# Kernel tuning notes

Hardware: AMD Instinct MI355X
Metric: run time of the kernel (lower is better)

The kernel has to match this reference:

```python
import jax, jax.numpy as jnp
import numpy as np

B, T, C, H = 2, 2048, 1024, 16
D = C // H  # head dim = 64

def setup_inputs() -> dict:
    key = jax.random.key(0)
    ks = jax.random.split(key, 5)
    s = 1.0 / np.sqrt(C)
    return {
        "x": jax.random.normal(ks[0], (B, T, C), jnp.float32),
        "Wq": jax.random.normal(ks[1], (C, C), jnp.float32) * s,
        "Wk": jax.random.normal(ks[2], (C, C), jnp.float32) * s,
        "Wv": jax.random.normal(ks[3], (C, C), jnp.float32) * s,
        "Wo": jax.random.normal(ks[4], (C, C), jnp.float32) * s,
    }

def reference(x, Wq, Wk, Wv, Wo):
    # torch Linear: y = x @ W.T  (weights stored [out, in])
    def proj(W):
        h = jnp.einsum('btc,oc->bto', x, W)
        return h.reshape(B, T, H, D).transpose(0, 2, 1, 3)  # [B,H,T,D]
    q, k, v = proj(Wq), proj(Wk), proj(Wv)
    scale = 1.0 / np.sqrt(D)
    att = jnp.einsum('bhqd,bhkd->bhqk', q, k) * scale  # [B,H,T,T]
    causal = jnp.tril(jnp.ones((T, T), bool))
    att = jnp.where(causal[None, None], att, -jnp.inf)
    att = jax.nn.softmax(att, axis=-1)
    y = jnp.einsum('bhqk,bhkd->bhqd', att, v)  # [B,H,T,D]
    y = y.transpose(0, 2, 1, 3).reshape(B, T, C)
    return jnp.einsum('btc,oc->bto', y, Wo)
```

## Files before the change

kernel.cpp:

```cpp
#include <hip/hip_runtime.h>
#include <math.h>

typedef short bf16x8 __attribute__((ext_vector_type(8)));
typedef float f32x4 __attribute__((ext_vector_type(4)));
typedef float f32x16 __attribute__((ext_vector_type(16)));
typedef int int2v __attribute__((ext_vector_type(2)));

constexpr int Bc = 2, Tc = 2048, Cc = 1024, Hc = 16, Dc = 64;
constexpr int Mc = Bc * Tc;

#if __has_builtin(__builtin_amdgcn_exp2f)
#define EXP2(x) __builtin_amdgcn_exp2f(x)
#else
#define EXP2(x) exp2f(x)
#endif

#define SBAR() do { asm volatile("" ::: "memory"); \
                    __builtin_amdgcn_s_barrier();   \
                    asm volatile("" ::: "memory"); } while (0)

__device__ __forceinline__ unsigned short f2bf(float f) {
    union { float f; unsigned u; } v; v.f = f;
    unsigned r = v.u + 0x7fffu + ((v.u >> 16) & 1u);
    return (unsigned short)(r >> 16);
}

__device__ __forceinline__ float bf2f(unsigned short u) {
    union { unsigned u; float f; } v; v.u = (unsigned)u << 16; return v.f;
}

__device__ __forceinline__ unsigned cvt_pk_bf16(float lo, float hi) {
    unsigned r;
    asm("v_cvt_pk_bf16_f32 %0, %1, %2" : "=v"(r) : "v"(lo), "v"(hi));
    return r;
}

__device__ __forceinline__ void gload16(const void* g, void* l) {
    __builtin_amdgcn_global_load_lds(
        (const __attribute__((address_space(1))) void*)g,
        (__attribute__((address_space(3))) void*)l, 16, 0, 0);
}

__global__ __launch_bounds__(256)
void cast_bf16(const float* __restrict__ in, unsigned short* __restrict__ out, int n8) {
    int i = blockIdx.x * 256 + threadIdx.x;
    if (i >= n8) return;
    const float4* p = (const float4*)in;
    float4 a = p[i * 2], b = p[i * 2 + 1];
    union { unsigned short u[8]; bf16x8 v; } r;
    r.u[0] = f2bf(a.x); r.u[1] = f2bf(a.y); r.u[2] = f2bf(a.z); r.u[3] = f2bf(a.w);
    r.u[4] = f2bf(b.x); r.u[5] = f2bf(b.y); r.u[6] = f2bf(b.z); r.u[7] = f2bf(b.w);
    *(bf16x8*)(out + i * 8) = r.v;
}

__global__ __launch_bounds__(256)
void cast_w4(const float* __restrict__ a, const float* __restrict__ b,
             const float* __restrict__ c, const float* __restrict__ d,
             unsigned short* __restrict__ oa, unsigned short* __restrict__ ob,
             unsigned short* __restrict__ oc, unsigned short* __restrict__ od) {
    const float* src = blockIdx.y == 0 ? a : blockIdx.y == 1 ? b : blockIdx.y == 2 ? c : d;
    unsigned short* dst = blockIdx.y == 0 ? oa : blockIdx.y == 1 ? ob : blockIdx.y == 2 ? oc : od;
    int i = blockIdx.x * 256 + threadIdx.x;
    const float4* p = (const float4*)src;
    float4 x = p[i * 2], y = p[i * 2 + 1];
    union { unsigned short u[8]; bf16x8 v; } r;
    r.u[0] = f2bf(x.x); r.u[1] = f2bf(x.y); r.u[2] = f2bf(x.z); r.u[3] = f2bf(x.w);
    r.u[4] = f2bf(y.x); r.u[5] = f2bf(y.y); r.u[6] = f2bf(y.z); r.u[7] = f2bf(y.w);
    *(bf16x8*)(dst + i * 8) = r.v;
}

__global__ __launch_bounds__(256)
void gemm_qkv(const unsigned short* __restrict__ A,
              const unsigned short* __restrict__ Wq,
              const unsigned short* __restrict__ Wk,
              const unsigned short* __restrict__ Wv,
              unsigned short* __restrict__ Qo,
              unsigned short* __restrict__ Ko,
              unsigned short* __restrict__ Vo) {
    __shared__ unsigned short As[128 * 32];
    __shared__ unsigned short Bs[64 * 32];
    const int t = threadIdx.x;
    const int lane = t & 63, l15 = lane & 15, l4 = lane >> 4;
    const int w = t >> 6, wr = w >> 1, wc = w & 1;
    const int seg = blockIdx.y >> 4;
    const unsigned short* W = seg == 0 ? Wq : seg == 1 ? Wk : Wv;
    const int m0 = blockIdx.x * 128, n0 = (blockIdx.y & 15) * 64;

    f32x4 acc[4][2] = {};

    for (int k0 = 0; k0 < Cc; k0 += 32) {
        __syncthreads();
        #pragma unroll
        for (int it = 0; it < 2; ++it) {
            int c = t + it * 256;
            int row = c >> 2, ko = (c & 3) << 3;
            gload16(A + (size_t)(m0 + row) * Cc + k0 + ko, As + c * 8);
        }
        {
            int row = t >> 2, ko = (t & 3) << 3;
            gload16(W + (size_t)(n0 + row) * Cc + k0 + ko, Bs + t * 8);
        }
        __syncthreads();
        bf16x8 af[4], bfr[2];
        #pragma unroll
        for (int i = 0; i < 4; ++i)
            af[i] = *(const bf16x8*)(As + ((wr * 64 + i * 16 + l15) * 32 + l4 * 8));
        #pragma unroll
        for (int j = 0; j < 2; ++j)
            bfr[j] = *(const bf16x8*)(Bs + ((wc * 32 + j * 16 + l15) * 32 + l4 * 8));
        #pragma unroll
        for (int i = 0; i < 4; ++i)
            #pragma unroll
            for (int j = 0; j < 2; ++j)
                acc[i][j] = __builtin_amdgcn_mfma_f32_16x16x32_bf16(af[i], bfr[j], acc[i][j], 0, 0, 0);
    }

    const float qscale = 0.18033688011112042f;
    const int r0 = wr * 64 + (l4 << 2);
    const int c0 = wc * 32 + l15;
    #pragma unroll
    for (int i = 0; i < 4; ++i)
        #pragma unroll
        for (int j = 0; j < 2; ++j)
            #pragma unroll
            for (int r = 0; r < 4; ++r) {
                int row = m0 + r0 + i * 16 + r;
                int col = n0 + c0 + j * 16;
                float v = acc[i][j][r];
                int bb = row >> 11, tt = row & (Tc - 1);
                int hh = col >> 6, dd = col & 63;
                if (seg == 0)
                    Qo[((((size_t)bb * Hc + hh) * Tc + tt) << 6) + dd] = f2bf(v * qscale);
                else if (seg == 1)
                    Ko[((((size_t)bb * Hc + hh) * Tc + tt) << 6) + dd] = f2bf(v);
                else
                    Vo[(((size_t)bb * Hc + hh) * Dc + dd) * Tc + tt] = f2bf(v);
            }
}

__global__ __launch_bounds__(256)
void gemm_out(const unsigned short* __restrict__ A,
              const unsigned short* __restrict__ W,
              float* __restrict__ outp) {
    __shared__ unsigned short As[64 * 32];
    __shared__ unsigned short Bs[64 * 32];
    const int t = threadIdx.x;
    const int lane = t & 63, l15 = lane & 15, l4 = lane >> 4;
    const int w = t >> 6, wr = w >> 1, wc = w & 1;
    const int m0 = blockIdx.x * 64, n0 = blockIdx.y * 64;

    f32x4 acc[2][2] = {};

    for (int k0 = 0; k0 < Cc; k0 += 32) {
        __syncthreads();
        {
            int row = t >> 2, ko = (t & 3) << 3;
            gload16(A + (size_t)(m0 + row) * Cc + k0 + ko, As + t * 8);
            gload16(W + (size_t)(n0 + row) * Cc + k0 + ko, Bs + t * 8);
        }
        __syncthreads();
        bf16x8 af[2], bfr[2];
        #pragma unroll
        for (int i = 0; i < 2; ++i)
            af[i] = *(const bf16x8*)(As + ((wr * 32 + i * 16 + l15) * 32 + l4 * 8));
        #pragma unroll
        for (int j = 0; j < 2; ++j)
            bfr[j] = *(const bf16x8*)(Bs + ((wc * 32 + j * 16 + l15) * 32 + l4 * 8));
        #pragma unroll
        for (int i = 0; i < 2; ++i)
            #pragma unroll
            for (int j = 0; j < 2; ++j)
                acc[i][j] = __builtin_amdgcn_mfma_f32_16x16x32_bf16(af[i], bfr[j], acc[i][j], 0, 0, 0);
    }

    const int r0 = wr * 32 + (l4 << 2);
    const int c0 = wc * 32 + l15;
    #pragma unroll
    for (int i = 0; i < 2; ++i)
        #pragma unroll
        for (int j = 0; j < 2; ++j)
            #pragma unroll
            for (int r = 0; r < 4; ++r)
                outp[(size_t)(m0 + r0 + i * 16 + r) * Cc + n0 + c0 + j * 16] = acc[i][j][r];
}

__device__ __constant__ unsigned char JOBS[48] = {
    159, 223, 222, 15, 158, 157, 221, 220, 14, 156,
    155, 219, 218, 13, 154, 153, 217, 216, 12, 152,
    151, 215, 214, 11, 150, 149, 213, 212, 10, 148,
    147, 211, 210,  9, 146, 145, 209, 208,  8, 144,
      7,   6,   5,  4,   3,   2,   1,   0
};

__global__ __launch_bounds__(128)
void attn_mfma(const unsigned short* __restrict__ Q,
               const unsigned short* __restrict__ K,
               const unsigned short* __restrict__ Vt,
               unsigned short* __restrict__ Y,
               unsigned short* __restrict__ P1,
               float* __restrict__ mlf) {
    __shared__ unsigned short Ks[2][64 * 64];
    __shared__ unsigned short Vs[2][64 * 64];

    const int t = threadIdx.x, lane = t & 63, w = t >> 6;
    const int l31 = lane & 31, h = lane >> 5;
    const int bh = blockIdx.x;
    const int bb = bh >> 4, hh = bh & 15;

    const unsigned char job = JOBS[blockIdx.y];
    const int c = job & 31;
    const bool split = job & 128;
    const int half = (job >> 6) & 1;
    const int ntile = c + 1, smid = ntile >> 1;
    const int kb0 = (split && half) ? smid : 0;
    const int kb1 = (split && !half) ? smid : ntile;

    const int qbase = c * 64 + w * 32;
    const int q = qbase + l31;

    const unsigned short* Qp = Q + (size_t)bh * Tc * Dc;
    const unsigned short* Kp = K + (size_t)bh * Tc * Dc;
    const unsigned short* Vp = Vt + (size_t)bh * Dc * Tc;

    bf16x8 qf[4];
    #pragma unroll
    for (int kc = 0; kc < 4; ++kc)
        qf[kc] = *(const bf16x8*)(Qp + (size_t)q * 64 + kc * 16 + h * 8);

    f32x16 ot[2] = {};
    float m = -INFINITY, lsum = 0.f;

    auto stage = [&](int kb, int buf) {
        #pragma unroll
        for (int it = 0; it < 4; ++it) {
            int idx = t + it * 128;
            int row = idx >> 3, slot = idx & 7;
            int ss = slot ^ (row & 7);
            gload16(Kp + (size_t)(kb * 64 + row) * 64 + ss * 8, &Ks[buf][idx * 8]);
            gload16(Vp + (size_t)row * Tc + kb * 64 + ss * 8, &Vs[buf][idx * 8]);
        }
    };

    stage(kb0, 0);
    if (kb0 + 1 < kb1) stage(kb0 + 1, 1);

    for (int kb = kb0; kb < kb1; ++kb) {
        const int cur = (kb - kb0) & 1;
        if (kb + 1 < kb1) asm volatile("s_waitcnt vmcnt(8)" ::: "memory");
        else              asm volatile("s_waitcnt vmcnt(0)" ::: "memory");
        SBAR();

        f32x16 st[2] = {};
        __builtin_amdgcn_s_setprio(1);
        #pragma unroll
        for (int nt = 0; nt < 2; ++nt) {
            int key = nt * 32 + l31;
            #pragma unroll
            for (int kc = 0; kc < 4; ++kc) {
                int boff = (kc * 32 + h * 16) ^ ((key & 7) << 4);
                bf16x8 kf = *(const bf16x8*)(&Ks[cur][((key << 7) + boff) >> 1]);
                st[nt] = __builtin_amdgcn_mfma_f32_32x32x16_bf16(kf, qf[kc], st[nt], 0, 0, 0);
            }
        }
        __builtin_amdgcn_s_setprio(0);

        if (kb * 64 + 63 > qbase) {
            #pragma unroll
            for (int nt = 0; nt < 2; ++nt)
                #pragma unroll
                for (int r = 0; r < 16; ++r) {
                    int key = kb * 64 + nt * 32 + (r & 3) + 8 * (r >> 2) + 4 * h;
                    if (key > q) st[nt][r] = -1e30f;
                }
        }

        float mx[16];
        #pragma unroll
        for (int r = 0; r < 16; ++r) mx[r] = fmaxf(st[0][r], st[1][r]);
        #pragma unroll
        for (int s2 = 8; s2 > 0; s2 >>= 1)
            #pragma unroll
            for (int r = 0; r < s2; ++r) mx[r] = fmaxf(mx[r], mx[r + s2]);
        float tmax = fmaxf(mx[0], __shfl_xor(mx[0], 32));

        if (__any(tmax > m + 8.f)) {
            float mn = fmaxf(m, tmax);
            float al = EXP2(m - mn);
            m = mn;
            lsum *= al;
            #pragma unroll
            for (int dt = 0; dt < 2; ++dt)
                #pragma unroll
                for (int r = 0; r < 16; ++r) ot[dt][r] *= al;
        }

        float psa[4] = {0.f, 0.f, 0.f, 0.f};
        #pragma unroll
        for (int nt = 0; nt < 2; ++nt)
            #pragma unroll
            for (int r = 0; r < 16; ++r) {
                float p = EXP2(st[nt][r] - m);
                st[nt][r] = p;
                psa[r & 3] += p;
            }
        lsum += (psa[0] + psa[1]) + (psa[2] + psa[3]);

        #pragma unroll
        for (int nt = 0; nt < 2; ++nt) {
            unsigned a0 = cvt_pk_bf16(st[nt][0],  st[nt][1]);
            unsigned b0 = cvt_pk_bf16(st[nt][4],  st[nt][5]);
            unsigned a1 = cvt_pk_bf16(st[nt][2],  st[nt][3]);
            unsigned b1 = cvt_pk_bf16(st[nt][6],  st[nt][7]);
            int2v r0 = __builtin_amdgcn_permlane32_swap((int)a0, (int)b0, false, false);
            int2v r1 = __builtin_amdgcn_permlane32_swap((int)a1, (int)b1, false, false);
            union { unsigned u[4]; bf16x8 v; } pf0, pf1;
            pf0.u[0] = r0.x; pf0.u[1] = r1.x; pf0.u[2] = r0.y; pf0.u[3] = r1.y;
            unsigned c0 = cvt_pk_bf16(st[nt][8],  st[nt][9]);
            unsigned d0 = cvt_pk_bf16(st[nt][12], st[nt][13]);
            unsigned c1 = cvt_pk_bf16(st[nt][10], st[nt][11]);
            unsigned d1 = cvt_pk_bf16(st[nt][14], st[nt][15]);
            int2v r2 = __builtin_amdgcn_permlane32_swap((int)c0, (int)d0, false, false);
            int2v r3 = __builtin_amdgcn_permlane32_swap((int)c1, (int)d1, false, false);
            pf1.u[0] = r2.x; pf1.u[1] = r3.x; pf1.u[2] = r2.y; pf1.u[3] = r3.y;

            __builtin_amdgcn_s_setprio(1);
            #pragma unroll
            for (int dt = 0; dt < 2; ++dt) {
                int d = dt * 32 + l31;
                int v0off = (nt * 64 + h * 16) ^ ((d & 7) << 4);
                bf16x8 vf0 = *(const bf16x8*)(&Vs[cur][((d << 7) + v0off) >> 1]);
                ot[dt] = __builtin_amdgcn_mfma_f32_32x32x16_bf16(vf0, pf0.v, ot[dt], 0, 0, 0);
            }
            #pragma unroll
            for (int dt = 0; dt < 2; ++dt) {
                int d = dt * 32 + l31;
                int v1off = (nt * 64 + 32 + h * 16) ^ ((d & 7) << 4);
                bf16x8 vf1 = *(const bf16x8*)(&Vs[cur][((d << 7) + v1off) >> 1]);
                ot[dt] = __builtin_amdgcn_mfma_f32_32x32x16_bf16(vf1, pf1.v, ot[dt], 0, 0, 0);
            }
            __builtin_amdgcn_s_setprio(0);
        }

        SBAR();
        if (kb + 2 < kb1) stage(kb + 2, cur);
    }

    float lf = lsum + __shfl_xor(lsum, 32);
    unsigned short* dst = (split && half) ? P1 : Y;
    float inv = split ? 1.f : 1.f / lf;
    size_t base = ((size_t)bb * Tc + q) * Cc + hh * 64;
    #pragma unroll
    for (int dt = 0; dt < 2; ++dt)
        #pragma unroll
        for (int rg = 0; rg < 4; ++rg) {
            int d0 = dt * 32 + rg * 8 + 4 * h;
            ushort4 s4;
            s4.x = f2bf(ot[dt][rg * 4 + 0] * inv);
            s4.y = f2bf(ot[dt][rg * 4 + 1] * inv);
            s4.z = f2bf(ot[dt][rg * 4 + 2] * inv);
            s4.w = f2bf(ot[dt][rg * 4 + 3] * inv);
            *(ushort4*)(dst + base + d0) = s4;
        }
    if (split && h == 0) {
        int ridx = bh * 1024 + (q - 1024);
        mlf[ridx + (half ? 65536 : 0)]     = m;
        mlf[ridx + (half ? 98304 : 32768)] = lf;
    }
}

__global__ __launch_bounds__(256)
void attn_combine(unsigned short* __restrict__ Y,
                  const unsigned short* __restrict__ P1,
                  const float* __restrict__ mlf) {
    int tid = blockIdx.x * 256 + threadIdx.x;
    int ridx = tid >> 3;
    int d0 = (tid & 7) * 8;
    int bh = ridx >> 10, qq = ridx & 1023;
    int bb = bh >> 4, hh = bh & 15;
    int q = 1024 + qq;
    size_t off = ((size_t)bb * Tc + q) * Cc + hh * 64 + d0;
    float m0 = mlf[ridx], l0 = mlf[ridx + 32768];
    float m1 = mlf[ridx + 65536], l1 = mlf[ridx + 98304];
    float M = fmaxf(m0, m1);
    float a0 = exp2f(m0 - M), a1 = exp2f(m1 - M);
    float inv = 1.f / (l0 * a0 + l1 * a1);
    union { unsigned short u[8]; bf16x8 v; } y0, y1, r;
    y0.v = *(const bf16x8*)(Y + off);
    y1.v = *(const bf16x8*)(P1 + off);
    #pragma unroll
    for (int j = 0; j < 8; ++j)
        r.u[j] = f2bf((bf2f(y0.u[j]) * a0 + bf2f(y1.u[j]) * a1) * inv);
    *(bf16x8*)(Y + off) = r.v;
}

extern "C" void kernel_launch(void* const* d_in, const int* in_sizes, int n_in,
                              void* d_out, int out_size, void* d_ws, size_t ws_size,
                              hipStream_t stream) {
    const float* x  = (const float*)d_in[0];
    const float* Wq = (const float*)d_in[1];
    const float* Wk = (const float*)d_in[2];
    const float* Wv = (const float*)d_in[3];
    const float* Wo = (const float*)d_in[4];

    unsigned short* ws = (unsigned short*)d_ws;
    const size_t nX = (size_t)Mc * Cc;
    const size_t nW = (size_t)Cc * Cc;
    size_t off = 0;
    unsigned short* xb  = ws + off; off += nX;
    unsigned short* Wqb = ws + off; off += nW;
    unsigned short* Wkb = ws + off; off += nW;
    unsigned short* Wvb = ws + off; off += nW;
    unsigned short* Wob = ws + off; off += nW;
    unsigned short* Qw  = ws + off; off += nX;
    unsigned short* Kw  = ws + off; off += nX;
    unsigned short* Vtw = ws + off; off += nX;
    unsigned short* Yb  = ws + off; off += nX;

    dim3 blk(256);
    cast_bf16<<<dim3((int)(nX / 8 / 256)), blk, 0, stream>>>(x, xb, (int)(nX / 8));
    cast_w4<<<dim3(512, 4), blk, 0, stream>>>(Wq, Wk, Wv, Wo, Wqb, Wkb, Wvb, Wob);

    gemm_qkv<<<dim3(Mc / 128, 48), blk, 0, stream>>>(xb, Wqb, Wkb, Wvb, Qw, Kw, Vtw);

    unsigned short* P1 = xb;
    float* mlf = (float*)Wqb;
    attn_mfma<<<dim3(Bc * Hc, 48), dim3(128), 0, stream>>>(Qw, Kw, Vtw, Yb, P1, mlf);
    attn_combine<<<dim3(1024), blk, 0, stream>>>(Yb, P1, mlf);

    gemm_out<<<dim3(Mc / 64, Cc / 64), blk, 0, stream>>>(Yb, Wob, (float*)d_out);
}
```

Baseline: 133.3 us.

## Split attention KV range into up to three parts and widen QKV GEMM tiles

The attention kernel now splits the causal KV range of each query tile into one, two or three partitions depending on tile depth. It launches 72 jobs per head ordered longest-first to balance work across CUs, and the combine kernel merges two or three partial outputs with their max/sum statistics. Separately, the QKV GEMM tile grows from 128x64 to 128x128 so each A tile is reused more and fewer blocks are launched. This adds extra partial-output traffic and combine work in exchange for better load balance, and it repurposes more workspace buffers (Wqb, Wvb) as scratch.

```diff
diff --git a/kernel.cpp b/kernel.cpp
--- a/kernel.cpp
+++ b/kernel.cpp
@@ -78,15 +78,15 @@
               unsigned short* __restrict__ Ko,
               unsigned short* __restrict__ Vo) {
     __shared__ unsigned short As[128 * 32];
-    __shared__ unsigned short Bs[64 * 32];
+    __shared__ unsigned short Bs[128 * 32];
     const int t = threadIdx.x;
     const int lane = t & 63, l15 = lane & 15, l4 = lane >> 4;
     const int w = t >> 6, wr = w >> 1, wc = w & 1;
-    const int seg = blockIdx.y >> 4;
+    const int seg = blockIdx.y >> 3;
     const unsigned short* W = seg == 0 ? Wq : seg == 1 ? Wk : Wv;
-    const int m0 = blockIdx.x * 128, n0 = (blockIdx.y & 15) * 64;
-
-    f32x4 acc[4][2] = {};
+    const int m0 = blockIdx.x * 128, n0 = (blockIdx.y & 7) * 128;
+
+    f32x4 acc[4][4] = {};
 
     for (int k0 = 0; k0 < Cc; k0 += 32) {
         __syncthreads();
@@ -95,33 +95,30 @@
             int c = t + it * 256;
             int row = c >> 2, ko = (c & 3) << 3;
             gload16(A + (size_t)(m0 + row) * Cc + k0 + ko, As + c * 8);
-        }
-        {
-            int row = t >> 2, ko = (t & 3) << 3;
-            gload16(W + (size_t)(n0 + row) * Cc + k0 + ko, Bs + t * 8);
+            gload16(W + (size_t)(n0 + row) * Cc + k0 + ko, Bs + c * 8);
         }
         __syncthreads();
-        bf16x8 af[4], bfr[2];
+        bf16x8 af[4], bfr[4];
         #pragma unroll
         for (int i = 0; i < 4; ++i)
             af[i] = *(const bf16x8*)(As + ((wr * 64 + i * 16 + l15) * 32 + l4 * 8));
         #pragma unroll
-        for (int j = 0; j < 2; ++j)
-            bfr[j] = *(const bf16x8*)(Bs + ((wc * 32 + j * 16 + l15) * 32 + l4 * 8));
+        for (int j = 0; j < 4; ++j)
+            bfr[j] = *(const bf16x8*)(Bs + ((wc * 64 + j * 16 + l15) * 32 + l4 * 8));
         #pragma unroll
         for (int i = 0; i < 4; ++i)
             #pragma unroll
-            for (int j = 0; j < 2; ++j)
+            for (int j = 0; j < 4; ++j)
                 acc[i][j] = __builtin_amdgcn_mfma_f32_16x16x32_bf16(af[i], bfr[j], acc[i][j], 0, 0, 0);
     }
 
     const float qscale = 0.18033688011112042f;
     const int r0 = wr * 64 + (l4 << 2);
-    const int c0 = wc * 32 + l15;
+    const int c0 = wc * 64 + l15;
     #pragma unroll
     for (int i = 0; i < 4; ++i)
         #pragma unroll
-        for (int j = 0; j < 2; ++j)
+        for (int j = 0; j < 4; ++j)
             #pragma unroll
             for (int r = 0; r < 4; ++r) {
                 int row = m0 + r0 + i * 16 + r;
@@ -184,12 +181,16 @@
                 outp[(size_t)(m0 + r0 + i * 16 + r) * Cc + n0 + c0 + j * 16] = acc[i][j][r];
 }
 
-__device__ __constant__ unsigned char JOBS[48] = {
-    159, 223, 222, 15, 158, 157, 221, 220, 14, 156,
-    155, 219, 218, 13, 154, 153, 217, 216, 12, 152,
-    151, 215, 214, 11, 150, 149, 213, 212, 10, 148,
-    147, 211, 210,  9, 146, 145, 209, 208,  8, 144,
-      7,   6,   5,  4,   3,   2,   1,   0
+__device__ __constant__ unsigned char JOBS[72] = {
+    125,126,122,
+    124,120,121,116,117,118,113,114,110,
+    112,108,109,104,105,106,101,102, 98,
+    100, 96, 97, 92, 93, 94, 89, 90, 86, 60, 61, 57, 28,
+     88, 84, 85, 80, 81, 82, 77, 78, 74, 56, 52, 53, 49, 24,
+     76, 72, 73, 68, 69, 70, 65, 66, 48, 44, 45, 41, 20,
+     64, 40, 36, 37, 33, 16,
+     32, 12,
+      8,  4,  0
 };
 
 __global__ __launch_bounds__(128)
@@ -198,6 +199,7 @@
                const unsigned short* __restrict__ Vt,
                unsigned short* __restrict__ Y,
                unsigned short* __restrict__ P1,
+               unsigned short* __restrict__ P2,
                float* __restrict__ mlf) {
     __shared__ unsigned short Ks[2][64 * 64];
     __shared__ unsigned short Vs[2][64 * 64];
@@ -208,12 +210,13 @@
     const int bb = bh >> 4, hh = bh & 15;
 
     const unsigned char job = JOBS[blockIdx.y];
-    const int c = job & 31;
-    const bool split = job & 128;
-    const int half = (job >> 6) & 1;
-    const int ntile = c + 1, smid = ntile >> 1;
-    const int kb0 = (split && half) ? smid : 0;
-    const int kb1 = (split && !half) ? smid : ntile;
+    const int c = job >> 2, p = job & 3;
+    const int n = c + 1;
+    const int npart = c < 8 ? 1 : (c < 16 ? 2 : 3);
+    int kb0, kb1;
+    if (npart == 1)      { kb0 = 0;               kb1 = n; }
+    else if (npart == 2) { kb0 = p ? n / 2 : 0;   kb1 = p ? n : n / 2; }
+    else                 { kb0 = p * n / 3;       kb1 = (p + 1) * n / 3; }
 
     const int qbase = c * 64 + w * 32;
     const int q = qbase + l31;
@@ -299,9 +302,9 @@
         for (int nt = 0; nt < 2; ++nt)
             #pragma unroll
             for (int r = 0; r < 16; ++r) {
-                float p = EXP2(st[nt][r] - m);
-                st[nt][r] = p;
-                psa[r & 3] += p;
+                float pv = EXP2(st[nt][r] - m);
+                st[nt][r] = pv;
+                psa[r & 3] += pv;
             }
         lsum += (psa[0] + psa[1]) + (psa[2] + psa[3]);
 
@@ -346,9 +349,16 @@
     }
 
     float lf = lsum + __shfl_xor(lsum, 32);
-    unsigned short* dst = (split && half) ? P1 : Y;
-    float inv = split ? 1.f : 1.f / lf;
-    size_t base = ((size_t)bb * Tc + q) * Cc + hh * 64;
+    unsigned short* dst;
+    size_t base;
+    if (npart == 1 || p == 0) {
+        dst = Y;  base = ((size_t)bb * Tc + q) * Cc + hh * 64;
+    } else if (p == 1) {
+        dst = P1; base = ((size_t)(bb * 1536 + (q - 512))) * Cc + hh * 64;
+    } else {
+        dst = P2; base = ((size_t)(bb * 1024 + (q - 1024))) * Cc + hh * 64;
+    }
+    float inv = (npart == 1) ? 1.f / lf : 1.f;
     #pragma unroll
     for (int dt = 0; dt < 2; ++dt)
         #pragma unroll
@@ -361,36 +371,53 @@
             s4.w = f2bf(ot[dt][rg * 4 + 3] * inv);
             *(ushort4*)(dst + base + d0) = s4;
         }
-    if (split && h == 0) {
-        int ridx = bh * 1024 + (q - 1024);
-        mlf[ridx + (half ? 65536 : 0)]     = m;
-        mlf[ridx + (half ? 98304 : 32768)] = lf;
+    if (npart > 1 && h == 0) {
+        int mi = p * 49152 + bh * 1536 + (q - 512);
+        mlf[mi]          = m;
+        mlf[147456 + mi] = lf;
     }
 }
 
 __global__ __launch_bounds__(256)
 void attn_combine(unsigned short* __restrict__ Y,
                   const unsigned short* __restrict__ P1,
+                  const unsigned short* __restrict__ P2,
                   const float* __restrict__ mlf) {
     int tid = blockIdx.x * 256 + threadIdx.x;
-    int ridx = tid >> 3;
-    int d0 = (tid & 7) * 8;
-    int bh = ridx >> 10, qq = ridx & 1023;
-    int bb = bh >> 4, hh = bh & 15;
-    int q = 1024 + qq;
-    size_t off = ((size_t)bb * Tc + q) * Cc + hh * 64 + d0;
-    float m0 = mlf[ridx], l0 = mlf[ridx + 32768];
-    float m1 = mlf[ridx + 65536], l1 = mlf[ridx + 98304];
-    float M = fmaxf(m0, m1);
+    int rowIdx = tid >> 7;
+    int col8 = (tid & 127) * 8;
+    int bb = rowIdx / 1536, qoff = rowIdx % 1536;
+    int q = 512 + qoff;
+    int hh = col8 >> 6;
+    int mi = (bb * 16 + hh) * 1536 + qoff;
+    bool three = q >= 1024;
+
+    float m0 = mlf[mi],          l0 = mlf[147456 + mi];
+    float m1 = mlf[49152 + mi],  l1 = mlf[196608 + mi];
+    float m2 = three ? mlf[98304 + mi]  : -INFINITY;
+    float l2 = three ? mlf[245760 + mi] : 0.f;
+
+    float M = fmaxf(fmaxf(m0, m1), m2);
     float a0 = exp2f(m0 - M), a1 = exp2f(m1 - M);
-    float inv = 1.f / (l0 * a0 + l1 * a1);
-    union { unsigned short u[8]; bf16x8 v; } y0, y1, r;
-    y0.v = *(const bf16x8*)(Y + off);
-    y1.v = *(const bf16x8*)(P1 + off);
+    float a2 = three ? exp2f(m2 - M) : 0.f;
+    float inv = 1.f / (l0 * a0 + l1 * a1 + l2 * a2);
+
+    size_t offY = ((size_t)(bb * Tc + q)) * Cc + col8;
+    size_t off1 = ((size_t)rowIdx) * Cc + col8;
+    union { unsigned short u[8]; bf16x8 v; } y0, y1, y2, r;
+    y0.v = *(const bf16x8*)(Y + offY);
+    y1.v = *(const bf16x8*)(P1 + off1);
+    if (three) {
+        size_t off2 = ((size_t)(bb * 1024 + (q - 1024))) * Cc + col8;
+        y2.v = *(const bf16x8*)(P2 + off2);
+    }
     #pragma unroll
-    for (int j = 0; j < 8; ++j)
-        r.u[j] = f2bf((bf2f(y0.u[j]) * a0 + bf2f(y1.u[j]) * a1) * inv);
-    *(bf16x8*)(Y + off) = r.v;
+    for (int j = 0; j < 8; ++j) {
+        float acc = bf2f(y0.u[j]) * a0 + bf2f(y1.u[j]) * a1;
+        if (three) acc += bf2f(y2.u[j]) * a2;
+        r.u[j] = f2bf(acc * inv);
+    }
+    *(bf16x8*)(Y + offY) = r.v;
 }
 
 extern "C" void kernel_launch(void* const* d_in, const int* in_sizes, int n_in,
@@ -420,12 +447,13 @@
     cast_bf16<<<dim3((int)(nX / 8 / 256)), blk, 0, stream>>>(x, xb, (int)(nX / 8));
     cast_w4<<<dim3(512, 4), blk, 0, stream>>>(Wq, Wk, Wv, Wo, Wqb, Wkb, Wvb, Wob);
 
-    gemm_qkv<<<dim3(Mc / 128, 48), blk, 0, stream>>>(xb, Wqb, Wkb, Wvb, Qw, Kw, Vtw);
+    gemm_qkv<<<dim3(Mc / 128, 24), blk, 0, stream>>>(xb, Wqb, Wkb, Wvb, Qw, Kw, Vtw);
 
     unsigned short* P1 = xb;
-    float* mlf = (float*)Wqb;
-    attn_mfma<<<dim3(Bc * Hc, 48), dim3(128), 0, stream>>>(Qw, Kw, Vtw, Yb, P1, mlf);
-    attn_combine<<<dim3(1024), blk, 0, stream>>>(Yb, P1, mlf);
+    unsigned short* P2 = Wqb;
+    float* mlf = (float*)Wvb;
+    attn_mfma<<<dim3(Bc * Hc, 72), dim3(128), 0, stream>>>(Qw, Kw, Vtw, Yb, P1, P2, mlf);
+    attn_combine<<<dim3(1536), blk, 0, stream>>>(Yb, P1, P2, mlf);
 
     gemm_out<<<dim3(Mc / 64, Cc / 64), blk, 0, stream>>>(Yb, Wob, (float*)d_out);
 }
```

After: 119.1 us. 10.6% less time.
